# Optimization experiments

Hardware: AMD Instinct MI355X
Metric: run time of the kernel (lower is better)

Reference implementation:

```python
import jax, jax.numpy as jnp
import numpy as np

N = 50000      # nodes
DEG = 16       # incoming edges per node
E = N * DEG    # edges
F = 256        # nfeat
H = 8          # heads
DH = 32        # nhid // nheads
ALPHA = 0.2    # LeakyReLU negative slope


def setup_inputs() -> dict:
    key = jax.random.key(0)
    ks = jax.random.split(key, 6)
    h = jax.random.normal(ks[0], (N, F), jnp.float32)
    # xavier_uniform-like scale for W (gain 1.414)
    lim_w = 1.414 * np.sqrt(6.0 / (F + DH))
    W = jax.random.uniform(ks[1], (H, F, DH), jnp.float32, -lim_w, lim_w)
    bW = jnp.zeros((H, DH), jnp.float32)
    lim_a = 1.414 * np.sqrt(6.0 / (2 * DH + 1))
    a_src = jax.random.uniform(ks[2], (H, DH), jnp.float32, -lim_a, lim_a)
    a_dst = jax.random.uniform(ks[3], (H, DH), jnp.float32, -lim_a, lim_a)
    a_bias = jnp.zeros((H,), jnp.float32)
    src = jax.random.randint(ks[4], (E,), 0, N, dtype=jnp.int32)
    # every node gets exactly DEG incoming edges (ensures non-empty mailbox)
    dst = jnp.repeat(jnp.arange(N, dtype=jnp.int32), DEG)
    return {"h": h, "W": W, "bW": bW, "a_src": a_src, "a_dst": a_dst,
            "a_bias": a_bias, "src": src, "dst": dst}


def reference(h, W, bW, a_src, a_dst, a_bias, src, dst):
    # per-head projection: Wh[n,h,d]
    Wh = jnp.einsum('nf,hfd->nhd', h, W) + bW
    # decomposed attention linear: a([Wh_src, Wh_dst]) = s1[src] + s2[dst] + b
    s1 = jnp.einsum('nhd,hd->nh', Wh, a_src)   # [N,H]
    s2 = jnp.einsum('nhd,hd->nh', Wh, a_dst)   # [N,H]
    e = jax.nn.leaky_relu(s1[src] + s2[dst] + a_bias, ALPHA)  # [E,H]
    # segment softmax over incoming edges per destination node
    m = jax.ops.segment_max(e, dst, num_segments=N)           # [N,H]
    ex = jnp.exp(e - m[dst])
    denom = jax.ops.segment_sum(ex, dst, num_segments=N)      # [N,H]
    attn = ex / denom[dst]                                    # [E,H]
    # weighted scatter-sum aggregation of source features
    hp = jax.ops.segment_sum(attn[:, :, None] * Wh[src], dst, num_segments=N)  # [N,H,DH]
    # concat heads (matches torch.cat over head outputs)
    return hp.reshape(N, H * DH)
```

## Files before the change

kernel.cpp:

```cpp
#include <hip/hip_runtime.h>

#define NNODES 50000
#define FEAT 256
#define NH 8
#define DHEAD 32
#define DEG 16
#define CDIM 256

typedef __attribute__((ext_vector_type(4))) float floatx4;
typedef __attribute__((ext_vector_type(8))) short shortx8;
typedef __attribute__((ext_vector_type(8))) unsigned short ushortx8;

__device__ __forceinline__ unsigned short f2bf(float f) {
  union { float f; unsigned u; } v; v.f = f;
  unsigned r = v.u + 0x7fffu + ((v.u >> 16) & 1u);
  return (unsigned short)(r >> 16);
}
__device__ __forceinline__ float bf2f(unsigned short b) {
  union { unsigned u; float f; } v; v.u = ((unsigned)b) << 16;
  return v.f;
}

__global__ __launch_bounds__(256) void convert_wt(
    const float* __restrict__ W, unsigned short* __restrict__ Wt2) {
  int t = blockIdx.x * 256 + threadIdx.x;
#pragma unroll
  for (int p = 0; p < 4; ++p) {
    int idx = t * 4 + p;
    int jj = idx & 7;
    int l = (idx >> 3) & 63;
    int kt = (idx >> 9) & 7;
    int cgrp = idx >> 12;
    int c = cgrp * 16 + (l & 15);
    int f = kt * 32 + ((l >> 4) << 3) + jj;
    Wt2[idx] = f2bf(W[(size_t)(c >> 5) * (FEAT * DHEAD) + (size_t)f * DHEAD + (c & 31)]);
  }
}

__global__ __launch_bounds__(256) void gemm_fused(
    const float* __restrict__ h, const unsigned short* __restrict__ Wt2,
    const float* __restrict__ bW, const float* __restrict__ a_src,
    const float* __restrict__ a_dst, const float* __restrict__ a_bias,
    unsigned short* __restrict__ Whb, float* __restrict__ s1g,
    float* __restrict__ s2g) {
  __shared__ unsigned short As2[8 * 4 * 64 * 8];
  const int tid = threadIdx.x;
  const int w = tid >> 6, lane = tid & 63;
  const int mrow = lane & 15, quad = lane >> 4;
  const int row0 = blockIdx.x * 64;

  {
    int grow = row0 + w * 16 + mrow;
    if (grow > NNODES - 1) grow = NNODES - 1;
    const float* hp = h + (size_t)grow * FEAT + quad * 8;
#pragma unroll
    for (int kt = 0; kt < 8; ++kt) {
      float4 v0 = *(const float4*)(hp + kt * 32);
      float4 v1 = *(const float4*)(hp + kt * 32 + 4);
      shortx8 a8;
      a8[0] = (short)f2bf(v0.x); a8[1] = (short)f2bf(v0.y);
      a8[2] = (short)f2bf(v0.z); a8[3] = (short)f2bf(v0.w);
      a8[4] = (short)f2bf(v1.x); a8[5] = (short)f2bf(v1.y);
      a8[6] = (short)f2bf(v1.z); a8[7] = (short)f2bf(v1.w);
      *(shortx8*)&As2[((kt * 4 + w) * 64 + lane) * 8] = a8;
    }
  }
  __syncthreads();

  floatx4 acc[4][4] = {};
#pragma unroll
  for (int kt = 0; kt < 8; ++kt) {
    shortx8 af[4], bfr[4];
#pragma unroll
    for (int ni = 0; ni < 4; ++ni) {
      int cgrp = w * 4 + ni;
      bfr[ni] = *(const shortx8*)&Wt2[((size_t)(cgrp * 8 + kt) * 64 + lane) * 8];
    }
#pragma unroll
    for (int mi = 0; mi < 4; ++mi)
      af[mi] = *(const shortx8*)&As2[((kt * 4 + mi) * 64 + lane) * 8];
#pragma unroll
    for (int mi = 0; mi < 4; ++mi)
#pragma unroll
      for (int ni = 0; ni < 4; ++ni)
        acc[mi][ni] = __builtin_amdgcn_mfma_f32_16x16x32_bf16(
            af[mi], bfr[ni], acc[mi][ni], 0, 0, 0);
  }

  float aw_s[4], aw_d[4], bias[4];
#pragma unroll
  for (int ni = 0; ni < 4; ++ni) {
    int col = w * 64 + ni * 16 + mrow;
    aw_s[ni] = a_src[col];
    aw_d[ni] = a_dst[col];
    bias[ni] = bW[col];
  }
  float ab0 = a_bias[w * 2], ab1 = a_bias[w * 2 + 1];
#pragma unroll
  for (int mi = 0; mi < 4; ++mi) {
#pragma unroll
    for (int ni = 0; ni < 4; ++ni) {
      int col = w * 64 + ni * 16 + mrow;
#pragma unroll
      for (int r = 0; r < 4; ++r) {
        int row = row0 + mi * 16 + quad * 4 + r;
        float val = acc[mi][ni][r] + bias[ni];
        acc[mi][ni][r] = val;
        if (row < NNODES) Whb[(size_t)row * CDIM + col] = f2bf(val);
      }
    }
#pragma unroll
    for (int r = 0; r < 4; ++r) {
      float s1h0 = acc[mi][0][r] * aw_s[0] + acc[mi][1][r] * aw_s[1];
      float s1h1 = acc[mi][2][r] * aw_s[2] + acc[mi][3][r] * aw_s[3];
      float s2h0 = acc[mi][0][r] * aw_d[0] + acc[mi][1][r] * aw_d[1];
      float s2h1 = acc[mi][2][r] * aw_d[2] + acc[mi][3][r] * aw_d[3];
#pragma unroll
      for (int off = 1; off < 16; off <<= 1) {
        s1h0 += __shfl_xor(s1h0, off, 64);
        s1h1 += __shfl_xor(s1h1, off, 64);
        s2h0 += __shfl_xor(s2h0, off, 64);
        s2h1 += __shfl_xor(s2h1, off, 64);
      }
      if (mrow == 0) {
        int row = row0 + mi * 16 + quad * 4 + r;
        if (row < NNODES) {
          float2 s1v; s1v.x = s1h0; s1v.y = s1h1;
          float2 s2v; s2v.x = s2h0 + ab0; s2v.y = s2h1 + ab1;
          *(float2*)&s1g[(size_t)row * NH + w * 2] = s1v;
          *(float2*)&s2g[(size_t)row * NH + w * 2] = s2v;
        }
      }
    }
  }
}

__global__ __launch_bounds__(256) void aggregate(
    const unsigned short* __restrict__ Whb, const float* __restrict__ s1g,
    const float* __restrict__ s2g, const int* __restrict__ src,
    float* __restrict__ out) {
  const int lane = threadIdx.x & 63;
  const int n = blockIdx.x * 4 + (threadIdx.x >> 6);
  const int half = lane >> 5;
  const int l32 = lane & 31;
  const int hsc = lane & 7;
  const int hacc = l32 >> 2;

  int s0 = src[(size_t)n * DEG + (lane & 15)];
  float s2v = s2g[(size_t)n * NH + hsc];

  int se0 = __shfl(s0, lane >> 3);
  int se1 = __shfl(s0, (lane >> 3) + 8);
  float s1a = s1g[(size_t)se0 * NH + hsc];
  float s1b = s1g[(size_t)se1 * NH + hsc];

  int rsrc[8];
#pragma unroll
  for (int t = 0; t < 8; ++t) rsrc[t] = __shfl(s0, 2 * t + half);
  ushortx8 vrow[8];
#pragma unroll
  for (int t = 0; t < 8; ++t)
    vrow[t] = *(const ushortx8*)&Whb[(size_t)rsrc[t] * CDIM + l32 * 8];

  float sc0 = s1a + s2v; sc0 = sc0 > 0.f ? sc0 : 0.2f * sc0;
  float sc1 = s1b + s2v; sc1 = sc1 > 0.f ? sc1 : 0.2f * sc1;
  float m = fmaxf(sc0, sc1);
  m = fmaxf(m, __shfl_xor(m, 8));
  m = fmaxf(m, __shfl_xor(m, 16));
  m = fmaxf(m, __shfl_xor(m, 32));
  float ex0 = __expf(sc0 - m), ex1 = __expf(sc1 - m);
  float sum = ex0 + ex1;
  sum += __shfl_xor(sum, 8);
  sum += __shfl_xor(sum, 16);
  sum += __shfl_xor(sum, 32);
  float inv = 1.f / sum;
  float w0 = ex0 * inv;
  float w1 = ex1 * inv;

  float wgt[8];
#pragma unroll
  for (int t = 0; t < 4; ++t) {
    int sl = ((2 * t + half) << 3) | hacc;
    wgt[t] = __shfl(w0, sl);
    wgt[t + 4] = __shfl(w1, sl);
  }

  float acc[8] = {0.f, 0.f, 0.f, 0.f, 0.f, 0.f, 0.f, 0.f};
#pragma unroll
  for (int t = 0; t < 8; ++t) {
    ushortx8 v = vrow[t];
    float w = wgt[t];
#pragma unroll
    for (int j = 0; j < 8; ++j) acc[j] += w * bf2f(v[j]);
  }

#pragma unroll
  for (int j = 0; j < 8; ++j) acc[j] += __shfl_xor(acc[j], 32);
  floatx4 o;
  o.x = half ? acc[4] : acc[0];
  o.y = half ? acc[5] : acc[1];
  o.z = half ? acc[6] : acc[2];
  o.w = half ? acc[7] : acc[3];
  __builtin_nontemporal_store(
      o, (floatx4*)&out[(size_t)n * CDIM + l32 * 8 + half * 4]);
}

extern "C" void kernel_launch(void* const* d_in, const int* in_sizes, int n_in,
                              void* d_out, int out_size, void* d_ws, size_t ws_size,
                              hipStream_t stream) {
  const float* h = (const float*)d_in[0];
  const float* W = (const float*)d_in[1];
  const float* bW = (const float*)d_in[2];
  const float* a_src = (const float*)d_in[3];
  const float* a_dst = (const float*)d_in[4];
  const float* a_bias = (const float*)d_in[5];
  const int* src = (const int*)d_in[6];
  float* out = (float*)d_out;

  unsigned short* Whb = (unsigned short*)d_ws;
  unsigned short* Wt2 = Whb + (size_t)NNODES * CDIM;
  float* s1g = (float*)(Wt2 + CDIM * FEAT);
  float* s2g = s1g + (size_t)NNODES * NH;

  convert_wt<<<64, 256, 0, stream>>>(W, Wt2);
  gemm_fused<<<(NNODES + 63) / 64, 256, 0, stream>>>(h, Wt2, bW, a_src, a_dst,
                                                     a_bias, Whb, s1g, s2g);
  aggregate<<<NNODES / 4, 256, 0, stream>>>(Whb, s1g, s2g, src, out);
}
```

Baseline: 198.8 us.

## Split aggregation column quarters across XCDs for L2 locality of gathered rows

The aggregate kernel now launches four times as many blocks, and each block handles one 64-column quarter of the feature row. The quarter is chosen from the XCD index (blockIdx & 7), so each XCD's L2 only ever caches one quarter of the Wh table. This is meant to shrink the random-gather working set per L2 and raise the hit rate. In exchange it recomputes the softmax scores four times per node, adds more cross-lane shuffle reductions and idles 3/4 of lanes on the store.

```diff
diff --git a/kernel.cpp b/kernel.cpp
--- a/kernel.cpp
+++ b/kernel.cpp
@@ -140,11 +140,15 @@
     const float* __restrict__ s2g, const int* __restrict__ src,
     float* __restrict__ out) {
   const int lane = threadIdx.x & 63;
-  const int n = blockIdx.x * 4 + (threadIdx.x >> 6);
-  const int half = lane >> 5;
-  const int l32 = lane & 31;
+  const int b = blockIdx.x;
+  const int xcd = b & 7;
+  const int q = xcd >> 1;
+  const int sub = ((b >> 3) << 1) | (xcd & 1);
+  const int n = sub * 4 + (threadIdx.x >> 6);
+  const int rowgrp = lane >> 3;
+  const int colpart = lane & 7;
   const int hsc = lane & 7;
-  const int hacc = l32 >> 2;
+  const int hq = q * 2 + (colpart >> 2);
 
   int s0 = src[(size_t)n * DEG + (lane & 15)];
   float s2v = s2g[(size_t)n * NH + hsc];
@@ -154,13 +158,11 @@
   float s1a = s1g[(size_t)se0 * NH + hsc];
   float s1b = s1g[(size_t)se1 * NH + hsc];
 
-  int rsrc[8];
-#pragma unroll
-  for (int t = 0; t < 8; ++t) rsrc[t] = __shfl(s0, 2 * t + half);
-  ushortx8 vrow[8];
-#pragma unroll
-  for (int t = 0; t < 8; ++t)
-    vrow[t] = *(const ushortx8*)&Whb[(size_t)rsrc[t] * CDIM + l32 * 8];
+  int r0 = __shfl(s0, rowgrp);
+  int r1 = __shfl(s0, 8 + rowgrp);
+  const size_t cbase = (size_t)q * 64 + colpart * 8;
+  ushortx8 v0 = *(const ushortx8*)&Whb[(size_t)r0 * CDIM + cbase];
+  ushortx8 v1 = *(const ushortx8*)&Whb[(size_t)r1 * CDIM + cbase];
 
   float sc0 = s1a + s2v; sc0 = sc0 > 0.f ? sc0 : 0.2f * sc0;
   float sc1 = s1b + s2v; sc1 = sc1 > 0.f ? sc1 : 0.2f * sc1;
@@ -177,32 +179,30 @@
   float w0 = ex0 * inv;
   float w1 = ex1 * inv;
 
-  float wgt[8];
-#pragma unroll
-  for (int t = 0; t < 4; ++t) {
-    int sl = ((2 * t + half) << 3) | hacc;
-    wgt[t] = __shfl(w0, sl);
-    wgt[t + 4] = __shfl(w1, sl);
-  }
-
-  float acc[8] = {0.f, 0.f, 0.f, 0.f, 0.f, 0.f, 0.f, 0.f};
-#pragma unroll
-  for (int t = 0; t < 8; ++t) {
-    ushortx8 v = vrow[t];
-    float w = wgt[t];
-#pragma unroll
-    for (int j = 0; j < 8; ++j) acc[j] += w * bf2f(v[j]);
-  }
-
-#pragma unroll
-  for (int j = 0; j < 8; ++j) acc[j] += __shfl_xor(acc[j], 32);
-  floatx4 o;
-  o.x = half ? acc[4] : acc[0];
-  o.y = half ? acc[5] : acc[1];
-  o.z = half ? acc[6] : acc[2];
-  o.w = half ? acc[7] : acc[3];
-  __builtin_nontemporal_store(
-      o, (floatx4*)&out[(size_t)n * CDIM + l32 * 8 + half * 4]);
+  float wgt0 = __shfl(w0, rowgrp * 8 + hq);
+  float wgt1 = __shfl(w1, rowgrp * 8 + hq);
+
+  float acc[8];
+#pragma unroll
+  for (int j = 0; j < 8; ++j)
+    acc[j] = wgt0 * bf2f(v0[j]) + wgt1 * bf2f(v1[j]);
+
+#pragma unroll
+  for (int j = 0; j < 8; ++j) {
+    acc[j] += __shfl_xor(acc[j], 8);
+    acc[j] += __shfl_xor(acc[j], 16);
+    acc[j] += __shfl_xor(acc[j], 32);
+  }
+
+  if (rowgrp < 2) {
+    floatx4 o;
+    o.x = rowgrp ? acc[4] : acc[0];
+    o.y = rowgrp ? acc[5] : acc[1];
+    o.z = rowgrp ? acc[6] : acc[2];
+    o.w = rowgrp ? acc[7] : acc[3];
+    __builtin_nontemporal_store(
+        o, (floatx4*)&out[(size_t)n * CDIM + cbase + rowgrp * 4]);
+  }
 }
 
 extern "C" void kernel_launch(void* const* d_in, const int* in_sizes, int n_in,
@@ -225,5 +225,5 @@
   convert_wt<<<64, 256, 0, stream>>>(W, Wt2);
   gemm_fused<<<(NNODES + 63) / 64, 256, 0, stream>>>(h, Wt2, bW, a_src, a_dst,
                                                      a_bias, Whb, s1g, s2g);
-  aggregate<<<NNODES / 4, 256, 0, stream>>>(Whb, s1g, s2g, src, out);
-}
+  aggregate<<<50000, 256, 0, stream>>>(Whb, s1g, s2g, src, out);
+}
```

Result: slower. 204.8 us (+3.0%).
